# Performance work log

Hardware: AMD Instinct MI355X
Metric: run time of the kernel (lower is better)

The kernel has to match this reference:

```python
import jax, jax.numpy as jnp
import numpy as np

H, TD, NUM_NODES = 128, 32, 256
B, N, T = 16, 256, 128


def sinusoidal_pe(t, h, dtype=jnp.float32):
    pos = jnp.arange(t, dtype=dtype)[:, None]                      # [T,1]
    div = jnp.exp(jnp.arange(0, h, 2, dtype=dtype) * (-np.log(10000.0) / h))
    pe = jnp.zeros((t, h), dtype=dtype)
    pe = pe.at[:, 0::2].set(jnp.sin(pos * div))
    pe = pe.at[:, 1::2].set(jnp.cos(pos * div))
    return pe                                                      # [T,H]


def setup_inputs() -> dict:
    key = jax.random.key(0)
    ks = jax.random.split(key, 20)
    lin = lambda k, i, o: jax.random.normal(k, (i, o), jnp.float32) / np.sqrt(i)
    return {
        "xf": jax.random.normal(ks[0], (B, N, T, H), jnp.float32),
        "ex": jax.random.normal(ks[1], (B, T, TD), jnp.float32),
        "nf": jax.random.randint(ks[2], (N,), 0, NUM_NODES),
        "mask": jax.random.randint(ks[3], (B, N, T, H), 0, 2).astype(bool),
        "W_in": lin(ks[4], 3 * H, H), "b_in": jnp.zeros((H,), jnp.float32),
        "W_t": lin(ks[5], TD, H), "b_t": jnp.zeros((H,), jnp.float32),
        "E_node": jax.random.normal(ks[6], (NUM_NODES, H), jnp.float32),
        "W_q": lin(ks[7], H, H), "b_q": jnp.zeros((H,), jnp.float32),
        "W_k": lin(ks[8], H, H), "b_k": jnp.zeros((H,), jnp.float32),
        "W_v": lin(ks[9], H, H), "b_v": jnp.zeros((H,), jnp.float32),
        "W_o": lin(ks[10], H, H), "b_o": jnp.zeros((H,), jnp.float32),
    }


def reference(xf, ex, nf, mask, W_in, b_in, W_t, b_t, E_node,
              W_q, b_q, W_k, b_k, W_v, b_v, W_o, b_o):
    b, n, t, h = xf.shape
    # pos-embed + concat(time, node embeds) + linear + GELU (exact erf, like torch F.gelu)
    pe = sinusoidal_pe(t, h, xf.dtype)                              # [T,H]
    time_e = (ex @ W_t + b_t)[:, None, :, :]                        # [B,1,T,H]
    node_e = E_node[nf][None, :, None, :]                           # [1,N,1,H]
    cat = jnp.concatenate([
        xf + pe,
        jnp.broadcast_to(time_e, (b, n, t, h)),
        jnp.broadcast_to(node_e, (b, n, t, h)),
    ], axis=-1)                                                     # [B,N,T,3H]
    x = jax.nn.gelu(cat @ W_in + b_in, approximate=False)           # [B,N,T,H]
    # attention over T per (B,N)
    q = x @ W_q + b_q
    k = x @ W_k + b_k
    v = x @ W_v + b_v
    scores = jnp.einsum('bnsh,bnth->bnst', q, k) * (1.0 / np.sqrt(h))
    A = jnp.nan_to_num(jax.nn.softmax(scores, axis=-1), nan=0.0)    # [B,N,T,T]
    # masked-confidence reduction (detached A in original)
    t_masking = jnp.all(mask, axis=-1)[:, :, None, :].astype(A.dtype)  # [B,N,1,T]
    conf = 1.0 - jnp.sum(jax.lax.stop_gradient(A) * t_masking, axis=-1)  # [B,N,T]
    rec = jnp.einsum('bnst,bnth->bnsh', A, v)                       # [B,N,T,H]
    rec = rec @ W_o + b_o
    return rec, conf
```

## Files before the change

kernel.cpp:

```cpp
#include <hip/hip_runtime.h>
#include <hip/hip_bf16.h>
#include <stdint.h>


typedef __bf16 bf16;
typedef __bf16 bf16x4 __attribute__((ext_vector_type(4)));
typedef __bf16 bf16x8 __attribute__((ext_vector_type(8)));
typedef float  f32x4  __attribute__((ext_vector_type(4)));

#define MFMA16(a, b, c) __builtin_amdgcn_mfma_f32_16x16x32_bf16((a), (b), (c), 0, 0, 0)

__device__ __forceinline__ int allBytesNonzero(unsigned v) {
    return ((v - 0x01010101u) & ~v & 0x80808080u) == 0u;
}

__device__ __forceinline__ bf16x8 cvt8(const float* p) {
    float4 f0 = *reinterpret_cast<const float4*>(p);
    float4 f1 = *reinterpret_cast<const float4*>(p + 4);
    bf16x8 r;
    r[0] = (bf16)f0.x; r[1] = (bf16)f0.y; r[2] = (bf16)f0.z; r[3] = (bf16)f0.w;
    r[4] = (bf16)f1.x; r[5] = (bf16)f1.y; r[6] = (bf16)f1.z; r[7] = (bf16)f1.w;
    return r;
}

__device__ __forceinline__ float gelu_erf(float v) {
    float x  = v * 0.70710678118654752f;
    float ax = fabsf(x);
    float t  = __builtin_amdgcn_rcpf(1.0f + 0.3275911f * ax);
    float p  = ((((1.061405429f * t - 1.453152027f) * t + 1.421413741f) * t
                 - 0.284496736f) * t + 0.254829592f) * t;
    float er = 1.0f - p * __expf(-ax * ax);
    er = copysignf(er, x);
    return 0.5f * v * (1.0f + er);
}

__global__ void prep_all(const float* __restrict__ W_in, const float* __restrict__ Wq,
                         const float* __restrict__ Wk, const float* __restrict__ bq,
                         const float* __restrict__ Wv, const float* __restrict__ Wo,
                         const float* __restrict__ bv, const float* __restrict__ bo,
                         const int* __restrict__ nf, const float* __restrict__ E_node,
                         bf16* __restrict__ wsW, bf16* __restrict__ mstore,
                         bf16* __restrict__ nstore, float* __restrict__ vvec,
                         float* __restrict__ bias2, float* __restrict__ npart)
{
    const int blk = blockIdx.x, t = threadIdx.x;
    if (blk < 128) {
        wsW[blk * 128 + (t ^ ((blk & 15) << 3))] = (bf16)W_in[t * 128 + blk];
    } else if (blk < 256) {
        const int a = blk - 128;
        __shared__ float wqa[128];
        wqa[t] = Wq[a * 128 + t];
        __syncthreads();
        float acc = 0.f;
        for (int k = 0; k < 128; ++k) acc += wqa[k] * Wk[t * 128 + k];
        mstore[a * 128 + (t ^ ((a & 15) << 3))] = (bf16)acc;
        if (a == 0) {
            float av = 0.f;
            for (int j = 0; j < 128; ++j) av += Wk[t * 128 + j] * bq[j];
            vvec[t] = av;
        }
    } else if (blk < 384) {
        const int h = blk - 256;
        __shared__ float wvh[128];
        wvh[t] = Wv[h * 128 + t];
        __syncthreads();
        float acc = 0.f;
        for (int j = 0; j < 128; ++j) acc += wvh[j] * Wo[j * 128 + t];
        nstore[t * 128 + (h ^ ((t & 15) << 3))] = (bf16)acc;
        if (h == 0) {
            float b2 = 0.f;
            for (int j = 0; j < 128; ++j) b2 += bv[j] * Wo[j * 128 + t];
            bias2[t] = b2 + bo[t];
        }
    } else {
        const int n = blk - 384;
        int node = nf[n];
        const float* e = E_node + node * 128;
        float acc = 0.f;
        for (int k = 0; k < 128; ++k) acc += e[k] * W_in[(256 + k) * 128 + t];
        npart[n * 128 + t] = acc;
    }
}

__global__ void prep_bias(const float* __restrict__ ex, const float* __restrict__ W_t,
                          const float* __restrict__ b_t, const float* __restrict__ W_in,
                          const float* __restrict__ b_in, float* __restrict__ biasT)
{
    const int bt = blockIdx.x;
    const int t = bt & 127;
    const int h = threadIdx.x;
    __shared__ float te[128];
    __shared__ float sn[64], cs[64];
    float v = b_t[h];
    const float* exr = ex + (size_t)bt * 32;
    for (int d = 0; d < 32; ++d) v += exr[d] * W_t[d * 128 + h];
    te[h] = v;
    if (h < 64) {
        const float ninv = -9.210340371976184f / 128.0f;
        float div = expf((float)(2 * h) * ninv);
        float ang = (float)t * div;
        sn[h] = sinf(ang);
        cs[h] = cosf(ang);
    }
    __syncthreads();
    float acc = b_in[h];
    for (int j = 0; j < 64; ++j)
        acc += sn[j] * W_in[(2 * j) * 128 + h] + cs[j] * W_in[(2 * j + 1) * 128 + h];
    for (int k = 0; k < 128; ++k) acc += te[k] * W_in[(128 + k) * 128 + h];
    biasT[(size_t)bt * 128 + h] = acc;
}

#define STAGE_ISSUE(REGS, SRC)                                                  \
    {                                                                           \
        _Pragma("unroll")                                                       \
        for (int i = 0; i < 4; ++i)                                             \
            REGS[i] = *reinterpret_cast<const bf16x8*>((SRC) + (tid + i * 512) * 8); \
    }
#define STAGE_WRITE(REGS, DST)                                                  \
    {                                                                           \
        _Pragma("unroll")                                                       \
        for (int i = 0; i < 4; ++i)                                             \
            *reinterpret_cast<bf16x8*>(&(DST)[(tid + i * 512) * 8]) = REGS[i];  \
    }

__global__ __launch_bounds__(512, 4) void fused_main(
    const float* __restrict__ xf, const unsigned char* __restrict__ mask,
    const bf16* __restrict__ wsW, const float* __restrict__ biasT,
    const float* __restrict__ npart, const float* __restrict__ vvec,
    const float* __restrict__ bias2, float* __restrict__ out)
{
    const bf16* W1T = wsW;
    const bf16* Mst = wsW + 16384;
    const bf16* Nst = wsW + 32768;

    __shared__ bf16 sA[16384];
    __shared__ bf16 sB[16384];
    __shared__ bf16 sT[8][16][40];
    __shared__ __align__(16) float sTm[128];
    __shared__ __align__(16) float sWt[128];

    const int bn = blockIdx.x;
    const int b  = bn >> 8;
    const int n  = bn & 255;
    const int tid  = (int)threadIdx.x;
    const int w    = tid >> 6;
    const int lane = tid & 63;
    const int c = lane & 15;
    const int g = lane >> 4;
    const int s0 = w << 4;

    const f32x4 FZ = {0.f, 0.f, 0.f, 0.f};
    bf16x8 stgA[4], stgB[4];
    bf16* patch = &sT[w][0][0];
    const int cx = c << 3;

    if (tid < 128) {
        const uint4* mp = reinterpret_cast<const uint4*>(mask + ((size_t)bn * 128 + tid) * 128);
        int ok = 1;
        #pragma unroll
        for (int i = 0; i < 8; ++i) {
            uint4 u = mp[i];
            ok &= allBytesNonzero(u.x) & allBytesNonzero(u.y)
                & allBytesNonzero(u.z) & allBytesNonzero(u.w);
        }
        sTm[tid] = ok ? 1.0f : 0.0f;
    }

    STAGE_ISSUE(stgA, W1T);
    STAGE_ISSUE(stgB, Mst);
    bf16x8 af[4];
    {
        const float* xfb = xf + (size_t)bn * 16384;
        #pragma unroll
        for (int kk = 0; kk < 4; ++kk)
            af[kk] = cvt8(xfb + (s0 + c) * 128 + kk * 32 + g * 8);
    }
    STAGE_WRITE(stgA, sA);
    STAGE_WRITE(stgB, sB);
    __syncthreads();

    bf16x8 xb[4];
    {
        const float* biasB = biasT + (size_t)b * 16384;
        const float* npRow = npart + n * 128;
        const int t = s0 + c;
        float bbr[8][4];
        #pragma unroll
        for (int ht = 0; ht < 8; ++ht) {
            const int hb = ht * 16 + g * 4;
            const float4 bb  = *reinterpret_cast<const float4*>(biasB + t * 128 + hb);
            const float4 np4 = *reinterpret_cast<const float4*>(npRow + hb);
            bbr[ht][0] = bb.x + np4.x; bbr[ht][1] = bb.y + np4.y;
            bbr[ht][2] = bb.z + np4.z; bbr[ht][3] = bb.w + np4.w;
        }
        f32x4 acc[8];
        #pragma unroll
        for (int ht = 0; ht < 8; ++ht) acc[ht] = FZ;
        __builtin_amdgcn_s_setprio(1);
        #pragma unroll
        for (int kk = 0; kk < 4; ++kk) {
            const int k0 = kk * 32 + g * 8;
            #pragma unroll
            for (int ht = 0; ht < 8; ++ht) {
                bf16x8 aw = *reinterpret_cast<const bf16x8*>(
                    &sA[(ht * 16 + c) * 128 + (k0 ^ cx)]);
                acc[ht] = MFMA16(aw, af[kk], acc[ht]);
            }
        }
        __builtin_amdgcn_s_setprio(0);
        bf16x4 pk[8];
        #pragma unroll
        for (int ht = 0; ht < 8; ++ht)
            #pragma unroll
            for (int r = 0; r < 4; ++r)
                pk[ht][r] = (bf16)gelu_erf(acc[ht][r] + bbr[ht][r]);
        #pragma unroll
        for (int kk = 0; kk < 4; ++kk) {
            *reinterpret_cast<bf16x4*>(patch + c * 40 + g * 4)      = pk[2 * kk];
            *reinterpret_cast<bf16x4*>(patch + c * 40 + 16 + g * 4) = pk[2 * kk + 1];
            xb[kk] = *reinterpret_cast<const bf16x8*>(patch + c * 40 + g * 8);
        }
    }
    __syncthreads();

    STAGE_ISSUE(stgA, Nst);
    {
        f32x4 acc[8];
        #pragma unroll
        for (int ht = 0; ht < 8; ++ht) acc[ht] = FZ;
        __builtin_amdgcn_s_setprio(1);
        #pragma unroll
        for (int kk = 0; kk < 4; ++kk) {
            const int k0 = kk * 32 + g * 8;
            #pragma unroll
            for (int ht = 0; ht < 8; ++ht) {
                bf16x8 aw = *reinterpret_cast<const bf16x8*>(
                    &sB[(ht * 16 + c) * 128 + (k0 ^ cx)]);
                acc[ht] = MFMA16(aw, xb[kk], acc[ht]);
            }
        }
        __builtin_amdgcn_s_setprio(0);
        const int t = s0 + c;
        #pragma unroll
        for (int ht = 0; ht < 8; ++ht) {
            bf16x4 pk;
            #pragma unroll
            for (int r = 0; r < 4; ++r) pk[r] = (bf16)acc[ht][r];
            *reinterpret_cast<bf16x4*>(&sA[t * 128 + ((ht * 16 + g * 4) ^ cx)]) = pk;
        }
        float wd = 0.f;
        #pragma unroll
        for (int kk = 0; kk < 4; ++kk) {
            const float4 vA = *reinterpret_cast<const float4*>(vvec + kk * 32 + g * 8);
            const float4 vB = *reinterpret_cast<const float4*>(vvec + kk * 32 + g * 8 + 4);
            wd += (float)xb[kk][0] * vA.x + (float)xb[kk][1] * vA.y
                + (float)xb[kk][2] * vA.z + (float)xb[kk][3] * vA.w
                + (float)xb[kk][4] * vB.x + (float)xb[kk][5] * vB.y
                + (float)xb[kk][6] * vB.z + (float)xb[kk][7] * vB.w;
        }
        wd += __shfl_xor(wd, 16);
        wd += __shfl_xor(wd, 32);
        if (g == 0) sWt[t] = wd;
    }
    __syncthreads();

    const float rs = 0.08838834764831845f;
    float invl = 1.f;
    bf16x8 xp[4];

    {
        f32x4 sc[8];
        #pragma unroll
        for (int rt = 0; rt < 8; ++rt) sc[rt] = FZ;
        __builtin_amdgcn_s_setprio(1);
        #pragma unroll
        for (int kk = 0; kk < 4; ++kk) {
            const int k0 = kk * 32 + g * 8;
            #pragma unroll
            for (int rt = 0; rt < 8; ++rt) {
                bf16x8 ay = *reinterpret_cast<const bf16x8*>(
                    &sA[(rt * 16 + c) * 128 + (k0 ^ cx)]);
                sc[rt] = MFMA16(ay, xb[kk], sc[rt]);
            }
        }
        __builtin_amdgcn_s_setprio(0);

        STAGE_WRITE(stgA, sB);

        float ls = 0.f, wsum = 0.f;
        #pragma unroll
        for (int rt = 0; rt < 8; ++rt) {
            const float4 wt4 = *reinterpret_cast<const float4*>(&sWt[rt * 16 + g * 4]);
            const float4 tm4 = *reinterpret_cast<const float4*>(&sTm[rt * 16 + g * 4]);
            const float wtr[4] = {wt4.x, wt4.y, wt4.z, wt4.w};
            const float tmr[4] = {tm4.x, tm4.y, tm4.z, tm4.w};
            #pragma unroll
            for (int r = 0; r < 4; ++r) {
                float p = __expf((sc[rt][r] + wtr[r]) * rs);
                sc[rt][r] = p;
                ls += p;
                wsum += p * tmr[r];
            }
        }
        ls   += __shfl_xor(ls, 16);   ls   += __shfl_xor(ls, 32);
        wsum += __shfl_xor(wsum, 16); wsum += __shfl_xor(wsum, 32);
        invl = __builtin_amdgcn_rcpf(ls);
        if (g == 0)
            out[(size_t)67108864 + (size_t)bn * 128 + s0 + c] = 1.0f - wsum * invl;
        bf16x4 pkP[8];
        #pragma unroll
        for (int rt = 0; rt < 8; ++rt)
            #pragma unroll
            for (int r = 0; r < 4; ++r) pkP[rt][r] = (bf16)sc[rt][r];
        #pragma unroll
        for (int kk = 0; kk < 4; ++kk) {
            *reinterpret_cast<bf16x4*>(patch + c * 40 + g * 4)      = pkP[2 * kk];
            *reinterpret_cast<bf16x4*>(patch + c * 40 + 16 + g * 4) = pkP[2 * kk + 1];
            xp[kk] = *reinterpret_cast<const bf16x8*>(patch + c * 40 + g * 8);
        }
    }
    __syncthreads();

    {
        f32x4 acc[8];
        #pragma unroll
        for (int ct = 0; ct < 8; ++ct) acc[ct] = FZ;
        __builtin_amdgcn_s_setprio(1);
        #pragma unroll
        for (int kk = 0; kk < 4; ++kk) {
            const int k0 = kk * 32 + g * 8;
            #pragma unroll
            for (int ct = 0; ct < 8; ++ct) {
                bf16x8 bw = *reinterpret_cast<const bf16x8*>(
                    &sB[(ct * 16 + c) * 128 + (k0 ^ cx)]);
                acc[ct] = MFMA16(xb[kk], bw, acc[ct]);
            }
        }
        __builtin_amdgcn_s_setprio(0);
        #pragma unroll
        for (int ct = 0; ct < 8; ++ct) {
            bf16x4 pk;
            #pragma unroll
            for (int r = 0; r < 4; ++r) pk[r] = (bf16)acc[ct][r];
            *reinterpret_cast<bf16x4*>(&sA[(ct * 16 + c) * 128 + ((s0 + g * 4) ^ cx)]) = pk;
        }
    }
    __syncthreads();

    {
        f32x4 rc[8];
        #pragma unroll
        for (int rt = 0; rt < 8; ++rt) rc[rt] = FZ;
        __builtin_amdgcn_s_setprio(1);
        #pragma unroll
        for (int kk = 0; kk < 4; ++kk) {
            const int k0 = kk * 32 + g * 8;
            #pragma unroll
            for (int rt = 0; rt < 8; ++rt) {
                bf16x8 avf = *reinterpret_cast<const bf16x8*>(
                    &sA[(rt * 16 + c) * 128 + (k0 ^ cx)]);
                rc[rt] = MFMA16(avf, xp[kk], rc[rt]);
            }
        }
        __builtin_amdgcn_s_setprio(0);
        float* outb = out + (size_t)bn * 16384 + (size_t)(s0 + c) * 128;
        #pragma unroll
        for (int rt = 0; rt < 8; ++rt) {
            const int hb = rt * 16 + g * 4;
            const float4 b2 = *reinterpret_cast<const float4*>(bias2 + hb);
            float4 v;
            v.x = rc[rt][0] * invl + b2.x;
            v.y = rc[rt][1] * invl + b2.y;
            v.z = rc[rt][2] * invl + b2.z;
            v.w = rc[rt][3] * invl + b2.w;
            *reinterpret_cast<float4*>(outb + hb) = v;
        }
    }
}

extern "C" void kernel_launch(void* const* d_in, const int* in_sizes, int n_in,
                              void* d_out, int out_size, void* d_ws, size_t ws_size,
                              hipStream_t stream)
{
    (void)in_sizes; (void)n_in; (void)out_size; (void)ws_size;
    const float* xf     = (const float*)d_in[0];
    const float* ex     = (const float*)d_in[1];
    const int*   nf     = (const int*)d_in[2];
    const unsigned char* mask = (const unsigned char*)d_in[3];
    const float* W_in   = (const float*)d_in[4];
    const float* b_in   = (const float*)d_in[5];
    const float* W_t    = (const float*)d_in[6];
    const float* b_t    = (const float*)d_in[7];
    const float* E_node = (const float*)d_in[8];
    const float* W_q    = (const float*)d_in[9];
    const float* b_q    = (const float*)d_in[10];
    const float* W_k    = (const float*)d_in[11];
    const float* b_k    = (const float*)d_in[12];
    const float* W_v    = (const float*)d_in[13];
    const float* b_v    = (const float*)d_in[14];
    const float* W_o    = (const float*)d_in[15];
    const float* b_o    = (const float*)d_in[16];
    (void)b_k;
    float* out = (float*)d_out;

    bf16*  wsW    = (bf16*)d_ws;
    bf16*  mstore = wsW + 16384;
    bf16*  nstore = wsW + 32768;
    float* biasT  = (float*)((char*)d_ws + 98304);
    float* npart  = (float*)((char*)d_ws + 1146880);
    float* vvec   = (float*)((char*)d_ws + 1277952);
    float* bias2  = (float*)((char*)d_ws + 1278464);

    prep_all<<<640, 128, 0, stream>>>(W_in, W_q, W_k, b_q, W_v, W_o, b_v, b_o,
                                      nf, E_node, wsW, mstore, nstore,
                                      vvec, bias2, npart);
    prep_bias<<<2048, 128, 0, stream>>>(ex, W_t, b_t, W_in, b_in, biasT);
    fused_main<<<4096, 512, 0, stream>>>(xf, mask, wsW, biasT, npart,
                                         vvec, bias2, out);
}
```

Measured before the change: 225.0 us.

## Read weights directly from global memory and drop shared staging buffer sB

Result: slower. 612.7 us (+172.3%).

```diff
diff --git a/kernel.cpp b/kernel.cpp
--- a/kernel.cpp
+++ b/kernel.cpp
@@ -110,20 +110,7 @@
     biasT[(size_t)bt * 128 + h] = acc;
 }
 
-#define STAGE_ISSUE(REGS, SRC)                                                  \
-    {                                                                           \
-        _Pragma("unroll")                                                       \
-        for (int i = 0; i < 4; ++i)                                             \
-            REGS[i] = *reinterpret_cast<const bf16x8*>((SRC) + (tid + i * 512) * 8); \
-    }
-#define STAGE_WRITE(REGS, DST)                                                  \
-    {                                                                           \
-        _Pragma("unroll")                                                       \
-        for (int i = 0; i < 4; ++i)                                             \
-            *reinterpret_cast<bf16x8*>(&(DST)[(tid + i * 512) * 8]) = REGS[i];  \
-    }
-
-__global__ __launch_bounds__(512, 4) void fused_main(
+__global__ __launch_bounds__(512, 6) void fused_main(
     const float* __restrict__ xf, const unsigned char* __restrict__ mask,
     const bf16* __restrict__ wsW, const float* __restrict__ biasT,
     const float* __restrict__ npart, const float* __restrict__ vvec,
@@ -134,7 +121,6 @@
     const bf16* Nst = wsW + 32768;
 
     __shared__ bf16 sA[16384];
-    __shared__ bf16 sB[16384];
     __shared__ bf16 sT[8][16][40];
     __shared__ __align__(16) float sTm[128];
     __shared__ __align__(16) float sWt[128];
@@ -150,7 +136,6 @@
     const int s0 = w << 4;
 
     const f32x4 FZ = {0.f, 0.f, 0.f, 0.f};
-    bf16x8 stgA[4], stgB[4];
     bf16* patch = &sT[w][0][0];
     const int cx = c << 3;
 
@@ -166,8 +151,6 @@
         sTm[tid] = ok ? 1.0f : 0.0f;
     }
 
-    STAGE_ISSUE(stgA, W1T);
-    STAGE_ISSUE(stgB, Mst);
     bf16x8 af[4];
     {
         const float* xfb = xf + (size_t)bn * 16384;
@@ -175,9 +158,6 @@
         for (int kk = 0; kk < 4; ++kk)
             af[kk] = cvt8(xfb + (s0 + c) * 128 + kk * 32 + g * 8);
     }
-    STAGE_WRITE(stgA, sA);
-    STAGE_WRITE(stgB, sB);
-    __syncthreads();
 
     bf16x8 xb[4];
     {
@@ -203,7 +183,7 @@
             #pragma unroll
             for (int ht = 0; ht < 8; ++ht) {
                 bf16x8 aw = *reinterpret_cast<const bf16x8*>(
-                    &sA[(ht * 16 + c) * 128 + (k0 ^ cx)]);
+                    &W1T[(ht * 16 + c) * 128 + (k0 ^ cx)]);
                 acc[ht] = MFMA16(aw, af[kk], acc[ht]);
             }
         }
@@ -221,9 +201,7 @@
             xb[kk] = *reinterpret_cast<const bf16x8*>(patch + c * 40 + g * 8);
         }
     }
-    __syncthreads();
-
-    STAGE_ISSUE(stgA, Nst);
+
     {
         f32x4 acc[8];
         #pragma unroll
@@ -235,7 +213,7 @@
             #pragma unroll
             for (int ht = 0; ht < 8; ++ht) {
                 bf16x8 aw = *reinterpret_cast<const bf16x8*>(
-                    &sB[(ht * 16 + c) * 128 + (k0 ^ cx)]);
+                    &Mst[(ht * 16 + c) * 128 + (k0 ^ cx)]);
                 acc[ht] = MFMA16(aw, xb[kk], acc[ht]);
             }
         }
@@ -267,6 +245,7 @@
     const float rs = 0.08838834764831845f;
     float invl = 1.f;
     bf16x8 xp[4];
+    bf16x4 vpk[8];
 
     {
         f32x4 sc[8];
@@ -285,7 +264,28 @@
         }
         __builtin_amdgcn_s_setprio(0);
 
-        STAGE_WRITE(stgA, sB);
+        {
+            f32x4 acc[8];
+            #pragma unroll
+            for (int ct = 0; ct < 8; ++ct) acc[ct] = FZ;
+            __builtin_amdgcn_s_setprio(1);
+            #pragma unroll
+            for (int kk = 0; kk < 4; ++kk) {
+                const int k0 = kk * 32 + g * 8;
+                #pragma unroll
+                for (int ct = 0; ct < 8; ++ct) {
+                    bf16x8 bw = *reinterpret_cast<const bf16x8*>(
+                        &Nst[(ct * 16 + c) * 128 + (k0 ^ cx)]);
+                    acc[ct] = MFMA16(xb[kk], bw, acc[ct]);
+                }
+            }
+            __builtin_amdgcn_s_setprio(0);
+            #pragma unroll
+            for (int ct = 0; ct < 8; ++ct)
+                #pragma unroll
+                for (int r = 0; r < 4; ++r)
+                    vpk[ct][r] = (bf16)acc[ct][r];
+        }
 
         float ls = 0.f, wsum = 0.f;
         #pragma unroll
@@ -322,28 +322,9 @@
     __syncthreads();
 
     {
-        f32x4 acc[8];
-        #pragma unroll
-        for (int ct = 0; ct < 8; ++ct) acc[ct] = FZ;
-        __builtin_amdgcn_s_setprio(1);
-        #pragma unroll
-        for (int kk = 0; kk < 4; ++kk) {
-            const int k0 = kk * 32 + g * 8;
-            #pragma unroll
-            for (int ct = 0; ct < 8; ++ct) {
-                bf16x8 bw = *reinterpret_cast<const bf16x8*>(
-                    &sB[(ct * 16 + c) * 128 + (k0 ^ cx)]);
-                acc[ct] = MFMA16(xb[kk], bw, acc[ct]);
-            }
-        }
-        __builtin_amdgcn_s_setprio(0);
-        #pragma unroll
-        for (int ct = 0; ct < 8; ++ct) {
-            bf16x4 pk;
-            #pragma unroll
-            for (int r = 0; r < 4; ++r) pk[r] = (bf16)acc[ct][r];
-            *reinterpret_cast<bf16x4*>(&sA[(ct * 16 + c) * 128 + ((s0 + g * 4) ^ cx)]) = pk;
-        }
+        #pragma unroll
+        for (int ct = 0; ct < 8; ++ct)
+            *reinterpret_cast<bf16x4*>(&sA[(ct * 16 + c) * 128 + ((s0 + g * 4) ^ cx)]) = vpk[ct];
     }
     __syncthreads();
 
```
